# Performance work log

Hardware: AMD Instinct MI355X
Metric: run time of the kernel (lower is better)

The kernel has to match this reference:

```python
import jax, jax.numpy as jnp
import numpy as np

T, N, E, IN_DIM, HID = 3, 100000, 1600000, 128, 64


def setup_inputs() -> dict:
    key = jax.random.key(0)
    ks = jax.random.split(key, 10)
    feats = jax.random.normal(ks[0], (T, N, IN_DIM), jnp.float32)
    src_seq = jax.random.randint(ks[1], (T, E), 0, N, dtype=jnp.int32)
    dst_seq = jax.random.randint(ks[2], (T, E), 0, N, dtype=jnp.int32)
    src_next = jax.random.randint(ks[3], (E,), 0, N, dtype=jnp.int32)
    dst_next = jax.random.randint(ks[4], (E,), 0, N, dtype=jnp.int32)
    init = lambda k, shp, fan: jax.random.normal(k, shp, jnp.float32) / np.float32(np.sqrt(fan))
    W1 = init(ks[5], (IN_DIM, HID), IN_DIM)
    W2 = init(ks[6], (HID, HID), HID)
    W3 = init(ks[7], (2 * HID, HID), 2 * HID)
    W4 = init(ks[8], (HID, 1), HID)
    b1 = jnp.zeros((HID,), jnp.float32)
    b2 = jnp.zeros((HID,), jnp.float32)
    b3 = jnp.zeros((HID,), jnp.float32)
    b4 = jnp.zeros((1,), jnp.float32)
    return dict(feats=feats, W1=W1, b1=b1, W2=W2, b2=b2, W3=W3, b3=b3, W4=W4, b4=b4,
                src_seq=src_seq, dst_seq=dst_seq, src_next=src_next, dst_next=dst_next)


def _gcn_layer(x, src, dst, W, b):
    # symmetric-normalized GCN conv: h_v = (1/sqrt(d_in(v))) * sum_{u->v} x_u/sqrt(d_out(u)) @ W + b
    ones = jnp.ones(src.shape, x.dtype)
    deg_out = jax.ops.segment_sum(ones, src, num_segments=N)
    deg_in = jax.ops.segment_sum(ones, dst, num_segments=N)
    norm_src = jax.lax.rsqrt(jnp.maximum(deg_out, 1.0))
    norm_dst = jax.lax.rsqrt(jnp.maximum(deg_in, 1.0))
    msg = (x * norm_src[:, None])[src]                      # [E, d] gather
    agg = jax.ops.segment_sum(msg, dst, num_segments=N)     # [N, d] scatter-add
    agg = agg * norm_dst[:, None]
    return agg @ W + b


def _encode(x, src, dst, W1, b1, W2, b2):
    h = jax.nn.relu(_gcn_layer(x, src, dst, W1, b1))
    return _gcn_layer(h, src, dst, W2, b2)


def reference(feats, W1, b1, W2, b2, W3, b3, W4, b4, src_seq, dst_seq, src_next, dst_next):
    # per-timestep GCN encode over the T=3 snapshots (vmapped)
    h_seq = jax.vmap(lambda x, s, d: _encode(x, s, d, W1, b1, W2, b2))(feats, src_seq, dst_seq)  # [T, N, HID]
    h = h_seq[-1]  # use_temporal=False -> h_seq[:, -1, :]
    # edge gather + concat + 2-layer MLP scorer
    e = jnp.concatenate([h[src_next], h[dst_next]], axis=1)  # [E, 2*HID]
    score = jax.nn.relu(e @ W3 + b3) @ W4 + b4               # [E, 1]
    return score.squeeze(-1)
```

## Files before the change

### kernel.cpp

```cpp
#include <hip/hip_runtime.h>
#include <hip/hip_bf16.h>
#include <hip/hip_fp16.h>

#define IN_DIM 128
#define HID 64
#define BIN_BS 8192
#define BINB 512

typedef __hip_bfloat16 bf16;
typedef _Float16 fp16;
typedef _Float16 h2 __attribute__((ext_vector_type(2)));
typedef _Float16 f16x8 __attribute__((ext_vector_type(8)));
typedef float f32x4 __attribute__((ext_vector_type(4)));

__device__ __forceinline__ float loadf(const void* p, size_t i, int isf) {
    if (isf) return ((const float*)p)[i];
    unsigned int u = ((const unsigned short*)p)[i];
    union { unsigned int b; float f; } c;
    c.b = u << 16;
    return c.f;
}

__device__ __forceinline__ float bf2f(unsigned short u) {
    union { unsigned int b; float f; } c;
    c.b = ((unsigned int)u) << 16;
    return c.f;
}

__global__ void detect_kernel(const unsigned short* __restrict__ feats, int* flag) {
    int lane = threadIdx.x;
    int bad = 0;
    for (int j = lane; j < 128; j += 64) {
        unsigned short u = feats[j];
        int expo = (u >> 7) & 0xFF;
        if (expo >= 141) bad = 1;
    }
    unsigned long long m = __ballot(bad);
    if (lane == 0) *flag = (__popcll(m) > 4) ? 1 : 0;
}

__global__ void zero_kernel(int* __restrict__ p, int n) {
    int i = blockIdx.x * blockDim.x + threadIdx.x;
    int stride = gridDim.x * blockDim.x;
    for (; i < n; i += stride) p[i] = 0;
}

__global__ void gcinit_kernel(int* __restrict__ gcursor, int B, int CAP) {
    int t = blockIdx.x * blockDim.x + threadIdx.x;
    if (t < B) gcursor[t] = t * CAP;
}

__global__ __launch_bounds__(512) void bin_kernel(const int* __restrict__ src,
                                                  const int* __restrict__ dst,
                                                  int* __restrict__ deg_out,
                                                  int* __restrict__ gcursor,
                                                  int* __restrict__ binned,
                                                  int E, int sh, int nb) {
    __shared__ int scnt[BINB];
    __shared__ int sloff[BINB];
    __shared__ int sgbase[BINB];
    __shared__ int stage[BIN_BS];
    __shared__ int stotal;
    int tid = threadIdx.x;
    for (int batch = blockIdx.x; batch < nb; batch += gridDim.x) {
        int base = batch * BIN_BS;
        scnt[tid] = 0;
        __syncthreads();
        int ent[16], bk[16];
#pragma unroll
        for (int j = 0; j < 16; ++j) {
            int idx = base + tid + j * 512;
            bool ok = idx < E;
            int s = ok ? src[idx] : 0;
            int d = ok ? dst[idx] : 0;
            int b = d >> 8;
            bk[j] = ok ? b : -1;
            ent[j] = ((d & 255) << sh) | s;
            if (ok) {
                atomicAdd(&deg_out[s], 1);
                atomicAdd(&scnt[b], 1);
            }
        }
        __syncthreads();
        int c = scnt[tid];
        scnt[tid] = 0;
        sloff[tid] = c;
        __syncthreads();
        for (int off = 1; off < 512; off <<= 1) {
            int add = (tid >= off) ? sloff[tid - off] : 0;
            __syncthreads();
            sloff[tid] += add;
            __syncthreads();
        }
        int incl = sloff[tid];
        if (tid == 511) stotal = incl;
        sloff[tid] = incl - c;
        if (c > 0) sgbase[tid] = atomicAdd(&gcursor[tid], c);
        __syncthreads();
#pragma unroll
        for (int j = 0; j < 16; ++j) {
            int b = bk[j];
            if (b >= 0) {
                int r = atomicAdd(&scnt[b], 1);
                stage[sloff[b] + r] = ent[j];
            }
        }
        __syncthreads();
        int tot = stotal;
        for (int i = tid; i < tot; i += 512) {
            int lo = 0, hi = BINB - 1;
            while (lo < hi) {
                int mid = (lo + hi + 1) >> 1;
                if (sloff[mid] <= i) lo = mid;
                else hi = mid - 1;
            }
            binned[sgbase[lo] + (i - sloff[lo])] = stage[i];
        }
        __syncthreads();
    }
}

__global__ __launch_bounds__(512) void bucket_scan_kernel(const int* __restrict__ gcursor,
                                                          int* __restrict__ bbase,
                                                          int* __restrict__ row_start,
                                                          int B, int CAP, int N) {
    __shared__ int part[512];
    int tid = threadIdx.x;
    int c = (tid < B) ? (gcursor[tid] - tid * CAP) : 0;
    part[tid] = c;
    __syncthreads();
    for (int off = 1; off < 512; off <<= 1) {
        int add = (tid >= off) ? part[tid - off] : 0;
        __syncthreads();
        part[tid] += add;
        __syncthreads();
    }
    if (tid < B) bbase[tid] = part[tid] - c;
    if (tid == 511) row_start[N] = part[511];
}

__global__ __launch_bounds__(256) void csr_build_kernel(const int* __restrict__ binned,
                                                        const int* __restrict__ gcursor,
                                                        const int* __restrict__ bbase,
                                                        int* __restrict__ row_start,
                                                        int* __restrict__ csr_src,
                                                        int N, int CAP, int sh) {
    __shared__ int lcnt[256];
    __shared__ int loff[256];
    int b = blockIdx.x;
    int tid = threadIdx.x;
    int rbase = b * CAP;
    int cnt = gcursor[b] - rbase;
    int obase = bbase[b];
    int n0 = b << 8;
    int mask = (1 << sh) - 1;
    lcnt[tid] = 0;
    __syncthreads();
    for (int i = tid; i < cnt; i += 256) {
        int e = binned[rbase + i];
        atomicAdd(&lcnt[e >> sh], 1);
    }
    __syncthreads();
    int c = lcnt[tid];
    lcnt[tid] = 0;
    loff[tid] = c;
    __syncthreads();
    for (int off = 1; off < 256; off <<= 1) {
        int add = (tid >= off) ? loff[tid - off] : 0;
        __syncthreads();
        loff[tid] += add;
        __syncthreads();
    }
    int incl = loff[tid];
    loff[tid] = incl - c;
    if (n0 + tid < N) row_start[n0 + tid] = obase + incl - c;
    __syncthreads();
    for (int i = tid; i < cnt; i += 256) {
        int e = binned[rbase + i];
        int dl = e >> sh;
        int r = atomicAdd(&lcnt[dl], 1);
        csr_src[obase + loff[dl] + r] = e & mask;
    }
}


__global__ __launch_bounds__(256) void xw1_mfma_kernel(const void* __restrict__ feats, size_t xoff,
                                                       const void* __restrict__ W1,
                                                       const int* __restrict__ deg_out,
                                                       const int* __restrict__ flag,
                                                       fp16* __restrict__ y1, int N) {
    __shared__ __align__(16) fp16 Wt[HID][IN_DIM + 8];
    int isf = *flag;
    int tid = threadIdx.x;
    for (int i = tid; i < IN_DIM * HID; i += 256) {
        int k = i >> 6, c = i & 63;
        Wt[c][k] = (fp16)loadf(W1, i, isf);
    }
    __syncthreads();
    int wave = tid >> 6, lane = tid & 63;
    int lr = lane & 15;
    int lk = (lane >> 4) * 8;
    f16x8 bfr[4][4];
#pragma unroll
    for (int ct = 0; ct < 4; ++ct)
#pragma unroll
        for (int kt = 0; kt < 4; ++kt)
            bfr[ct][kt] = *(const f16x8*)&Wt[ct * 16 + lr][kt * 32 + lk];
    int tb = blockIdx.x * 64 + wave * 16;
    int rc = min(tb + lr, N - 1);
    f16x8 afr[4];
    if (isf) {
        const float* xr = (const float*)feats + xoff + (size_t)rc * IN_DIM + lk;
#pragma unroll
        for (int kt = 0; kt < 4; ++kt) {
            float4 p0 = *(const float4*)(xr + kt * 32);
            float4 p1 = *(const float4*)(xr + kt * 32 + 4);
            f16x8 a;
            a[0] = (fp16)p0.x; a[1] = (fp16)p0.y; a[2] = (fp16)p0.z; a[3] = (fp16)p0.w;
            a[4] = (fp16)p1.x; a[5] = (fp16)p1.y; a[6] = (fp16)p1.z; a[7] = (fp16)p1.w;
            afr[kt] = a;
        }
    } else {
        const unsigned short* xr = (const unsigned short*)feats + xoff + (size_t)rc * IN_DIM + lk;
#pragma unroll
        for (int kt = 0; kt < 4; ++kt) {
            uint4 q = *(const uint4*)(xr + kt * 32);
            f16x8 a;
            a[0] = (fp16)bf2f((unsigned short)(q.x & 0xffff));
            a[1] = (fp16)bf2f((unsigned short)(q.x >> 16));
            a[2] = (fp16)bf2f((unsigned short)(q.y & 0xffff));
            a[3] = (fp16)bf2f((unsigned short)(q.y >> 16));
            a[4] = (fp16)bf2f((unsigned short)(q.z & 0xffff));
            a[5] = (fp16)bf2f((unsigned short)(q.z >> 16));
            a[6] = (fp16)bf2f((unsigned short)(q.w & 0xffff));
            a[7] = (fp16)bf2f((unsigned short)(q.w >> 16));
            afr[kt] = a;
        }
    }
    f32x4 acc[4] = {};
#pragma unroll
    for (int ct = 0; ct < 4; ++ct)
#pragma unroll
        for (int kt = 0; kt < 4; ++kt)
            acc[ct] = __builtin_amdgcn_mfma_f32_16x16x32_f16(afr[kt], bfr[ct][kt], acc[ct], 0, 0, 0);
    int sr0 = tb + (lane >> 4) * 4;
    int sc = lane & 15;
#pragma unroll
    for (int i = 0; i < 4; ++i) {
        int row = sr0 + i;
        if (row < N) {
            float ns = rsqrtf(fmaxf((float)deg_out[row], 1.f));
#pragma unroll
            for (int ct = 0; ct < 4; ++ct)
                y1[(size_t)row * HID + ct * 16 + sc] = (fp16)(acc[ct][i] * ns);
        }
    }
}

__global__ __launch_bounds__(256) void mlp2_mfma_kernel(const fp16* __restrict__ h,
                                                        const void* __restrict__ W2,
                                                        const int* __restrict__ deg_out,
                                                        const int* __restrict__ flag,
                                                        fp16* __restrict__ y2, int N) {
    __shared__ __align__(16) fp16 Wt[HID][HID + 8];
    int isf = *flag;
    int tid = threadIdx.x;
    for (int i = tid; i < HID * HID; i += 256) {
        int k = i >> 6, c = i & 63;
        Wt[c][k] = (fp16)loadf(W2, i, isf);
    }
    __syncthreads();
    int wave = tid >> 6, lane = tid & 63;
    int lr = lane & 15, lk = (lane >> 4) * 8;
    f16x8 bfr[4][2];
#pragma unroll
    for (int ct = 0; ct < 4; ++ct)
#pragma unroll
        for (int kt = 0; kt < 2; ++kt)
            bfr[ct][kt] = *(const f16x8*)&Wt[ct * 16 + lr][kt * 32 + lk];
    int tb = blockIdx.x * 64 + wave * 16;
    int rc = min(tb + lr, N - 1);
    f16x8 afr[2];
#pragma unroll
    for (int kt = 0; kt < 2; ++kt)
        afr[kt] = *(const f16x8*)&h[(size_t)rc * HID + kt * 32 + lk];
    f32x4 acc[4] = {};
#pragma unroll
    for (int ct = 0; ct < 4; ++ct)
#pragma unroll
        for (int kt = 0; kt < 2; ++kt)
            acc[ct] = __builtin_amdgcn_mfma_f32_16x16x32_f16(afr[kt], bfr[ct][kt], acc[ct], 0, 0, 0);
    int sr0 = tb + (lane >> 4) * 4;
    int sc = lane & 15;
#pragma unroll
    for (int i = 0; i < 4; ++i) {
        int row = sr0 + i;
        if (row < N) {
            float ns = rsqrtf(fmaxf((float)deg_out[row], 1.f));
#pragma unroll
            for (int ct = 0; ct < 4; ++ct)
                y2[(size_t)row * HID + ct * 16 + sc] = (fp16)(acc[ct][i] * ns);
        }
    }
}

__global__ __launch_bounds__(256) void mlp3_mfma_kernel(const fp16* __restrict__ h,
                                                        const void* __restrict__ W3,
                                                        const int* __restrict__ flag,
                                                        fp16* __restrict__ u,
                                                        fp16* __restrict__ v, int N) {
    __shared__ __align__(16) fp16 Wt[HID][2 * HID + 8];
    int isf = *flag;
    int tid = threadIdx.x;
    for (int i = tid; i < 2 * HID * HID; i += 256) {
        int k = i >> 6, c = i & 63;
        Wt[c][k] = (fp16)loadf(W3, i, isf);
    }
    __syncthreads();
    int wave = tid >> 6, lane = tid & 63;
    int lr = lane & 15, lk = (lane >> 4) * 8;
    f16x8 bu[4][2], bv[4][2];
#pragma unroll
    for (int ct = 0; ct < 4; ++ct)
#pragma unroll
        for (int kt = 0; kt < 2; ++kt) {
            bu[ct][kt] = *(const f16x8*)&Wt[ct * 16 + lr][kt * 32 + lk];
            bv[ct][kt] = *(const f16x8*)&Wt[ct * 16 + lr][HID + kt * 32 + lk];
        }
    int tb = blockIdx.x * 64 + wave * 16;
    int rc = min(tb + lr, N - 1);
    f16x8 afr[2];
#pragma unroll
    for (int kt = 0; kt < 2; ++kt)
        afr[kt] = *(const f16x8*)&h[(size_t)rc * HID + kt * 32 + lk];
    f32x4 accu[4] = {}, accv[4] = {};
#pragma unroll
    for (int ct = 0; ct < 4; ++ct)
#pragma unroll
        for (int kt = 0; kt < 2; ++kt) {
            accu[ct] = __builtin_amdgcn_mfma_f32_16x16x32_f16(afr[kt], bu[ct][kt], accu[ct], 0, 0, 0);
            accv[ct] = __builtin_amdgcn_mfma_f32_16x16x32_f16(afr[kt], bv[ct][kt], accv[ct], 0, 0, 0);
        }
    int sr0 = tb + (lane >> 4) * 4;
    int sc = lane & 15;
#pragma unroll
    for (int i = 0; i < 4; ++i) {
        int row = sr0 + i;
        if (row < N) {
#pragma unroll
            for (int ct = 0; ct < 4; ++ct) {
                u[(size_t)row * HID + ct * 16 + sc] = (fp16)accu[ct][i];
                v[(size_t)row * HID + ct * 16 + sc] = (fp16)accv[ct][i];
            }
        }
    }
}

__global__ __launch_bounds__(256, 4) void gather_kernel(const fp16* __restrict__ y,
                                                        const void* __restrict__ bias,
                                                        const int* __restrict__ row_start,
                                                        const int* __restrict__ csr_src,
                                                        const int* __restrict__ flag,
                                                        fp16* __restrict__ h,
                                                        int N, int do_relu) {
    int isf = *flag;
    int tid = threadIdx.x;
    int wave = tid >> 6, lane = tid & 63;
    int half = lane >> 5, sub = lane & 31;
    float bl0 = loadf(bias, 2 * sub, isf), bl1 = loadf(bias, 2 * sub + 1, isf);
    const int NP = (N + 1) >> 1;
    for (int p = blockIdx.x * 4 + wave; p < NP; p += gridDim.x * 4) {
        int n = min(2 * p + half, N - 1);
        int rs = row_start[n];
        int re = row_start[n + 1];
        float a0 = 0.f, a1 = 0.f;
        for (int base_e = rs; base_e < re; base_e += 16) {
            int sarr[16];
#pragma unroll
            for (int j = 0; j < 16; ++j) {
                int ec = min(base_e + j, re - 1);
                sarr[j] = csr_src[ec];
            }
            unsigned uarr[16];
#pragma unroll
            for (int j = 0; j < 16; ++j)
                uarr[j] = ((const unsigned*)(y + (size_t)sarr[j] * HID))[sub];
#pragma unroll
            for (int j = 0; j < 16; ++j) {
                bool ok = base_e + j < re;
                h2 hh = __builtin_bit_cast(h2, uarr[j]);
                a0 += ok ? (float)hh[0] : 0.f;
                a1 += ok ? (float)hh[1] : 0.f;
            }
        }
        float nd = rsqrtf(fmaxf((float)(re - rs), 1.f));
        float r0 = fmaf(a0, nd, bl0);
        float r1 = fmaf(a1, nd, bl1);
        if (do_relu) { r0 = fmaxf(r0, 0.f); r1 = fmaxf(r1, 0.f); }
        if (2 * p + half < N) {
            h2 rr; rr[0] = (fp16)r0; rr[1] = (fp16)r1;
            ((unsigned*)(h + (size_t)n * HID))[sub] = __builtin_bit_cast(unsigned, rr);
        }
    }
}

#define SCORE_U 8
__global__ __launch_bounds__(256, 8) void score_kernel(const fp16* __restrict__ u,
                                                       const fp16* __restrict__ v,
                                                       const int* __restrict__ sn,
                                                       const int* __restrict__ dn,
                                                       const void* __restrict__ b3,
                                                       const void* __restrict__ W4,
                                                       const void* __restrict__ b4,
                                                       const int* __restrict__ flag,
                                                       void* __restrict__ out, int E) {
    int isf = *flag;
    int tid = threadIdx.x;
    int lane = tid & 63;
    int half = lane >> 5, sub = lane & 31;
    int gw = (blockIdx.x * 256 + tid) >> 6;
    int nw = gridDim.x * 4;
    float b30 = loadf(b3, 2 * sub, isf), b31 = loadf(b3, 2 * sub + 1, isf);
    float w40 = loadf(W4, 2 * sub, isf), w41 = loadf(W4, 2 * sub + 1, isf);
    float b4v = loadf(b4, 0, isf);
    const int P = (E + 1) >> 1;

    int p0 = gw;
    for (; p0 + (SCORE_U - 1) * nw < P - 1; p0 += SCORE_U * nw) {
        int ss[SCORE_U], dd[SCORE_U];
#pragma unroll
        for (int j = 0; j < SCORE_U; ++j) {
            int e = 2 * (p0 + j * nw) + half;
            ss[j] = sn[e];
            dd[j] = dn[e];
        }
        unsigned pu[SCORE_U], pv[SCORE_U];
#pragma unroll
        for (int j = 0; j < SCORE_U; ++j) {
            pu[j] = ((const unsigned*)(u + (size_t)ss[j] * HID))[sub];
            pv[j] = ((const unsigned*)(v + (size_t)dd[j] * HID))[sub];
        }
#pragma unroll
        for (int j = 0; j < SCORE_U; ++j) {
            int e = 2 * (p0 + j * nw) + half;
            h2 hu = __builtin_bit_cast(h2, pu[j]);
            h2 hv = __builtin_bit_cast(h2, pv[j]);
            float h0 = fmaxf((float)hu[0] + (float)hv[0] + b30, 0.f);
            float h1 = fmaxf((float)hu[1] + (float)hv[1] + b31, 0.f);
            float pp = fmaf(h0, w40, h1 * w41);
#pragma unroll
            for (int off = 16; off > 0; off >>= 1) pp += __shfl_xor(pp, off, 64);
            if (sub == 0) {
                float r = pp + b4v;
                if (isf) ((float*)out)[e] = r;
                else     ((bf16*)out)[e] = __float2bfloat16(r);
            }
        }
    }
    for (; p0 < P; p0 += nw) {
        int e = 2 * p0 + half;
        int ec = min(e, E - 1);
        int s = sn[ec], d = dn[ec];
        unsigned pu = ((const unsigned*)(u + (size_t)s * HID))[sub];
        unsigned pv = ((const unsigned*)(v + (size_t)d * HID))[sub];
        h2 hu = __builtin_bit_cast(h2, pu);
        h2 hv = __builtin_bit_cast(h2, pv);
        float h0 = fmaxf((float)hu[0] + (float)hv[0] + b30, 0.f);
        float h1 = fmaxf((float)hu[1] + (float)hv[1] + b31, 0.f);
        float pp = fmaf(h0, w40, h1 * w41);
#pragma unroll
        for (int off = 16; off > 0; off >>= 1) pp += __shfl_xor(pp, off, 64);
        if (sub == 0 && e < E) {
            float r = pp + b4v;
            if (isf) ((float*)out)[e] = r;
            else     ((bf16*)out)[e] = __float2bfloat16(r);
        }
    }
}

extern "C" void kernel_launch(void* const* d_in, const int* in_sizes, int n_in,
                              void* d_out, int out_size, void* d_ws, size_t ws_size,
                              hipStream_t stream) {
    const void* feats = d_in[0];
    const void* W1 = d_in[1];
    const void* b1 = d_in[2];
    const void* W2 = d_in[3];
    const void* b2 = d_in[4];
    const void* W3 = d_in[5];
    const void* b3 = d_in[6];
    const void* W4 = d_in[7];
    const void* b4 = d_in[8];
    const int* src_seq = (const int*)d_in[9];
    const int* dst_seq = (const int*)d_in[10];
    const int* src_next = (const int*)d_in[11];
    const int* dst_next = (const int*)d_in[12];

    const int E = in_sizes[11];
    const int N = in_sizes[0] / (3 * IN_DIM);
    const int T = in_sizes[9] / E;

    const size_t xoff = (size_t)(T - 1) * N * IN_DIM;
    const int* src = src_seq + (size_t)(T - 1) * E;
    const int* dst = dst_seq + (size_t)(T - 1) * E;

    char* w = (char*)d_ws;
    auto alloc = [&](size_t bytes) {
        void* p = (void*)w;
        w += (bytes + 255) & ~(size_t)255;
        return p;
    };
    int* flag      = (int*)alloc(4);
    int* deg_out   = (int*)alloc((size_t)N * 4);
    int* row_start = (int*)alloc((size_t)(N + 1) * 4);
    int* gcursor   = (int*)alloc(512 * 4);
    int* bbase     = (int*)alloc(512 * 4);
    int* csr_src   = (int*)alloc((size_t)E * 4);
    fp16* y1       = (fp16*)alloc((size_t)N * HID * 2);
    fp16* y2       = (fp16*)alloc((size_t)N * HID * 2);
    fp16* vv       = (fp16*)alloc((size_t)N * HID * 2);
    fp16* hbuf     = (fp16*)alloc((size_t)N * HID * 2);
    fp16* uu       = y1;
    int* binned    = (int*)y2;

    const int B = (N + 255) >> 8;
    int sh = 1;
    while ((1 << sh) < N) ++sh;
    int avg = (E + B - 1) / B;
    int CAP = (avg + avg / 2 + 256 + 15) & ~15;
    size_t maxints = (size_t)N * HID * 2 / 4;
    if ((size_t)B * CAP > maxints) CAP = (int)(maxints / B) & ~15;
    const int nb = (E + BIN_BS - 1) / BIN_BS;
    const int GB = (N + 63) / 64;

    detect_kernel<<<1, 64, 0, stream>>>((const unsigned short*)feats, flag);
    zero_kernel<<<512, 256, 0, stream>>>(deg_out, N);
    gcinit_kernel<<<2, 256, 0, stream>>>(gcursor, B, CAP);
    bin_kernel<<<nb, 512, 0, stream>>>(src, dst, deg_out, gcursor, binned, E, sh, nb);
    bucket_scan_kernel<<<1, 512, 0, stream>>>(gcursor, bbase, row_start, B, CAP, N);
    csr_build_kernel<<<B, 256, 0, stream>>>(binned, gcursor, bbase, row_start, csr_src,
                                            N, CAP, sh);
    xw1_mfma_kernel<<<GB, 256, 0, stream>>>(feats, xoff, W1, deg_out, flag, y1, N);
    gather_kernel<<<4096, 256, 0, stream>>>(y1, b1, row_start, csr_src, flag, hbuf, N, 1);
    mlp2_mfma_kernel<<<GB, 256, 0, stream>>>(hbuf, W2, deg_out, flag, y2, N);
    gather_kernel<<<4096, 256, 0, stream>>>(y2, b2, row_start, csr_src, flag, hbuf, N, 0);
    mlp3_mfma_kernel<<<GB, 256, 0, stream>>>(hbuf, W3, flag, uu, vv, N);
    score_kernel<<<4096, 256, 0, stream>>>(uu, vv, src_next, dst_next, b3, W4, b4, flag,
                                           (void*)d_out, E);
}
```

Before: 540.6 us.

## Fuse CSR neighbor gather into following MFMA matmul kernels

Each neighbor-aggregation gather is merged with the dense matmul that consumes it. The aggregated rows are staged in shared memory instead of being written to an intermediate global buffer and read back. This removes two kernel launches and the global round trip of an N×64 fp16 buffer. The separate zero and cursor-init kernels are also merged into one. In exchange, the gather now uses a fixed grid of 64-node blocks rather than a grid-stride loop, which changes load balance, and LDS use per block grows.

```diff
diff --git a/kernel.cpp b/kernel.cpp
--- a/kernel.cpp
+++ b/kernel.cpp
@@ -39,15 +39,12 @@
     if (lane == 0) *flag = (__popcll(m) > 4) ? 1 : 0;
 }
 
-__global__ void zero_kernel(int* __restrict__ p, int n) {
+__global__ void init_kernel(int* __restrict__ deg_out, int N,
+                            int* __restrict__ gcursor, int B, int CAP) {
     int i = blockIdx.x * blockDim.x + threadIdx.x;
     int stride = gridDim.x * blockDim.x;
-    for (; i < n; i += stride) p[i] = 0;
-}
-
-__global__ void gcinit_kernel(int* __restrict__ gcursor, int B, int CAP) {
-    int t = blockIdx.x * blockDim.x + threadIdx.x;
-    if (t < B) gcursor[t] = t * CAP;
+    for (int j = i; j < N; j += stride) deg_out[j] = 0;
+    if (i < B) gcursor[i] = i * CAP;
 }
 
 __global__ __launch_bounds__(512) void bin_kernel(const int* __restrict__ src,
@@ -257,20 +254,61 @@
     }
 }
 
-__global__ __launch_bounds__(256) void mlp2_mfma_kernel(const fp16* __restrict__ h,
-                                                        const void* __restrict__ W2,
-                                                        const int* __restrict__ deg_out,
-                                                        const int* __restrict__ flag,
-                                                        fp16* __restrict__ y2, int N) {
+__device__ __forceinline__ void half_gather(const fp16* __restrict__ y,
+                                            const int* __restrict__ csr_src,
+                                            int rs, int re, int sub,
+                                            float& a0, float& a1) {
+    for (int be = rs; be < re; be += 16) {
+        int sarr[16];
+#pragma unroll
+        for (int j = 0; j < 16; ++j)
+            sarr[j] = csr_src[min(be + j, re - 1)];
+        unsigned uarr[16];
+#pragma unroll
+        for (int j = 0; j < 16; ++j)
+            uarr[j] = ((const unsigned*)(y + (size_t)sarr[j] * HID))[sub];
+#pragma unroll
+        for (int j = 0; j < 16; ++j) {
+            bool ok = be + j < re;
+            h2 hh = __builtin_bit_cast(h2, uarr[j]);
+            a0 += ok ? (float)hh[0] : 0.f;
+            a1 += ok ? (float)hh[1] : 0.f;
+        }
+    }
+}
+
+__global__ __launch_bounds__(256, 4) void gmlp2_kernel(const fp16* __restrict__ y,
+                                                       const void* __restrict__ bias,
+                                                       const int* __restrict__ row_start,
+                                                       const int* __restrict__ csr_src,
+                                                       const void* __restrict__ W2,
+                                                       const int* __restrict__ deg_out,
+                                                       const int* __restrict__ flag,
+                                                       fp16* __restrict__ y2, int N) {
     __shared__ __align__(16) fp16 Wt[HID][HID + 8];
+    __shared__ __align__(16) unsigned hh[64][36];
     int isf = *flag;
     int tid = threadIdx.x;
     for (int i = tid; i < HID * HID; i += 256) {
         int k = i >> 6, c = i & 63;
         Wt[c][k] = (fp16)loadf(W2, i, isf);
     }
-    __syncthreads();
-    int wave = tid >> 6, lane = tid & 63;
+    int wave = tid >> 6, lane = tid & 63, half = lane >> 5, sub = lane & 31;
+    float bl0 = loadf(bias, 2 * sub, isf), bl1 = loadf(bias, 2 * sub + 1, isf);
+    int base_n = blockIdx.x * 64;
+    for (int it = 0; it < 8; ++it) {
+        int slot = it * 8 + wave * 2 + half;
+        int n = min(base_n + slot, N - 1);
+        int rs = row_start[n], re = row_start[n + 1];
+        float a0 = 0.f, a1 = 0.f;
+        half_gather(y, csr_src, rs, re, sub, a0, a1);
+        float nd = rsqrtf(fmaxf((float)(re - rs), 1.f));
+        h2 rr;
+        rr[0] = (fp16)fmaxf(fmaf(a0, nd, bl0), 0.f);
+        rr[1] = (fp16)fmaxf(fmaf(a1, nd, bl1), 0.f);
+        hh[slot][sub] = __builtin_bit_cast(unsigned, rr);
+    }
+    __syncthreads();
     int lr = lane & 15, lk = (lane >> 4) * 8;
     f16x8 bfr[4][2];
 #pragma unroll
@@ -278,18 +316,17 @@
 #pragma unroll
         for (int kt = 0; kt < 2; ++kt)
             bfr[ct][kt] = *(const f16x8*)&Wt[ct * 16 + lr][kt * 32 + lk];
-    int tb = blockIdx.x * 64 + wave * 16;
-    int rc = min(tb + lr, N - 1);
     f16x8 afr[2];
 #pragma unroll
     for (int kt = 0; kt < 2; ++kt)
-        afr[kt] = *(const f16x8*)&h[(size_t)rc * HID + kt * 32 + lk];
+        afr[kt] = *(const f16x8*)&hh[wave * 16 + lr][kt * 16 + (lk >> 1)];
     f32x4 acc[4] = {};
 #pragma unroll
     for (int ct = 0; ct < 4; ++ct)
 #pragma unroll
         for (int kt = 0; kt < 2; ++kt)
             acc[ct] = __builtin_amdgcn_mfma_f32_16x16x32_f16(afr[kt], bfr[ct][kt], acc[ct], 0, 0, 0);
+    int tb = base_n + wave * 16;
     int sr0 = tb + (lane >> 4) * 4;
     int sc = lane & 15;
 #pragma unroll
@@ -304,102 +341,90 @@
     }
 }
 
-__global__ __launch_bounds__(256) void mlp3_mfma_kernel(const fp16* __restrict__ h,
-                                                        const void* __restrict__ W3,
-                                                        const int* __restrict__ flag,
-                                                        fp16* __restrict__ u,
-                                                        fp16* __restrict__ v, int N) {
+__global__ __launch_bounds__(256, 4) void gmlp3_kernel(const fp16* __restrict__ y,
+                                                       const void* __restrict__ bias,
+                                                       const int* __restrict__ row_start,
+                                                       const int* __restrict__ csr_src,
+                                                       const void* __restrict__ W3,
+                                                       const int* __restrict__ flag,
+                                                       fp16* __restrict__ u,
+                                                       fp16* __restrict__ v, int N) {
     __shared__ __align__(16) fp16 Wt[HID][2 * HID + 8];
+    __shared__ __align__(16) unsigned hh[64][36];
     int isf = *flag;
     int tid = threadIdx.x;
     for (int i = tid; i < 2 * HID * HID; i += 256) {
         int k = i >> 6, c = i & 63;
         Wt[c][k] = (fp16)loadf(W3, i, isf);
     }
-    __syncthreads();
-    int wave = tid >> 6, lane = tid & 63;
+    int wave = tid >> 6, lane = tid & 63, half = lane >> 5, sub = lane & 31;
+    float bl0 = loadf(bias, 2 * sub, isf), bl1 = loadf(bias, 2 * sub + 1, isf);
+    int base_n = blockIdx.x * 64;
+    for (int it = 0; it < 8; ++it) {
+        int slot = it * 8 + wave * 2 + half;
+        int n = min(base_n + slot, N - 1);
+        int rs = row_start[n], re = row_start[n + 1];
+        float a0 = 0.f, a1 = 0.f;
+        half_gather(y, csr_src, rs, re, sub, a0, a1);
+        float nd = rsqrtf(fmaxf((float)(re - rs), 1.f));
+        h2 rr;
+        rr[0] = (fp16)fmaf(a0, nd, bl0);
+        rr[1] = (fp16)fmaf(a1, nd, bl1);
+        hh[slot][sub] = __builtin_bit_cast(unsigned, rr);
+    }
+    __syncthreads();
     int lr = lane & 15, lk = (lane >> 4) * 8;
-    f16x8 bu[4][2], bv[4][2];
-#pragma unroll
-    for (int ct = 0; ct < 4; ++ct)
-#pragma unroll
-        for (int kt = 0; kt < 2; ++kt) {
-            bu[ct][kt] = *(const f16x8*)&Wt[ct * 16 + lr][kt * 32 + lk];
-            bv[ct][kt] = *(const f16x8*)&Wt[ct * 16 + lr][HID + kt * 32 + lk];
-        }
-    int tb = blockIdx.x * 64 + wave * 16;
-    int rc = min(tb + lr, N - 1);
     f16x8 afr[2];
 #pragma unroll
     for (int kt = 0; kt < 2; ++kt)
-        afr[kt] = *(const f16x8*)&h[(size_t)rc * HID + kt * 32 + lk];
-    f32x4 accu[4] = {}, accv[4] = {};
-#pragma unroll
-    for (int ct = 0; ct < 4; ++ct)
-#pragma unroll
-        for (int kt = 0; kt < 2; ++kt) {
-            accu[ct] = __builtin_amdgcn_mfma_f32_16x16x32_f16(afr[kt], bu[ct][kt], accu[ct], 0, 0, 0);
-            accv[ct] = __builtin_amdgcn_mfma_f32_16x16x32_f16(afr[kt], bv[ct][kt], accv[ct], 0, 0, 0);
-        }
+        afr[kt] = *(const f16x8*)&hh[wave * 16 + lr][kt * 16 + (lk >> 1)];
+    int tb = base_n + wave * 16;
     int sr0 = tb + (lane >> 4) * 4;
     int sc = lane & 15;
-#pragma unroll
-    for (int i = 0; i < 4; ++i) {
-        int row = sr0 + i;
-        if (row < N) {
-#pragma unroll
-            for (int ct = 0; ct < 4; ++ct) {
-                u[(size_t)row * HID + ct * 16 + sc] = (fp16)accu[ct][i];
-                v[(size_t)row * HID + ct * 16 + sc] = (fp16)accv[ct][i];
+    {
+        f16x8 bu[4][2];
+#pragma unroll
+        for (int ct = 0; ct < 4; ++ct)
+#pragma unroll
+            for (int kt = 0; kt < 2; ++kt)
+                bu[ct][kt] = *(const f16x8*)&Wt[ct * 16 + lr][kt * 32 + lk];
+        f32x4 accu[4] = {};
+#pragma unroll
+        for (int ct = 0; ct < 4; ++ct)
+#pragma unroll
+            for (int kt = 0; kt < 2; ++kt)
+                accu[ct] = __builtin_amdgcn_mfma_f32_16x16x32_f16(afr[kt], bu[ct][kt], accu[ct], 0, 0, 0);
+#pragma unroll
+        for (int i = 0; i < 4; ++i) {
+            int row = sr0 + i;
+            if (row < N) {
+#pragma unroll
+                for (int ct = 0; ct < 4; ++ct)
+                    u[(size_t)row * HID + ct * 16 + sc] = (fp16)accu[ct][i];
             }
         }
     }
-}
-
-__global__ __launch_bounds__(256, 4) void gather_kernel(const fp16* __restrict__ y,
-                                                        const void* __restrict__ bias,
-                                                        const int* __restrict__ row_start,
-                                                        const int* __restrict__ csr_src,
-                                                        const int* __restrict__ flag,
-                                                        fp16* __restrict__ h,
-                                                        int N, int do_relu) {
-    int isf = *flag;
-    int tid = threadIdx.x;
-    int wave = tid >> 6, lane = tid & 63;
-    int half = lane >> 5, sub = lane & 31;
-    float bl0 = loadf(bias, 2 * sub, isf), bl1 = loadf(bias, 2 * sub + 1, isf);
-    const int NP = (N + 1) >> 1;
-    for (int p = blockIdx.x * 4 + wave; p < NP; p += gridDim.x * 4) {
-        int n = min(2 * p + half, N - 1);
-        int rs = row_start[n];
-        int re = row_start[n + 1];
-        float a0 = 0.f, a1 = 0.f;
-        for (int base_e = rs; base_e < re; base_e += 16) {
-            int sarr[16];
-#pragma unroll
-            for (int j = 0; j < 16; ++j) {
-                int ec = min(base_e + j, re - 1);
-                sarr[j] = csr_src[ec];
+    {
+        f16x8 bv[4][2];
+#pragma unroll
+        for (int ct = 0; ct < 4; ++ct)
+#pragma unroll
+            for (int kt = 0; kt < 2; ++kt)
+                bv[ct][kt] = *(const f16x8*)&Wt[ct * 16 + lr][HID + kt * 32 + lk];
+        f32x4 accv[4] = {};
+#pragma unroll
+        for (int ct = 0; ct < 4; ++ct)
+#pragma unroll
+            for (int kt = 0; kt < 2; ++kt)
+                accv[ct] = __builtin_amdgcn_mfma_f32_16x16x32_f16(afr[kt], bv[ct][kt], accv[ct], 0, 0, 0);
+#pragma unroll
+        for (int i = 0; i < 4; ++i) {
+            int row = sr0 + i;
+            if (row < N) {
+#pragma unroll
+                for (int ct = 0; ct < 4; ++ct)
+                    v[(size_t)row * HID + ct * 16 + sc] = (fp16)accv[ct][i];
             }
-            unsigned uarr[16];
-#pragma unroll
-            for (int j = 0; j < 16; ++j)
-                uarr[j] = ((const unsigned*)(y + (size_t)sarr[j] * HID))[sub];
-#pragma unroll
-            for (int j = 0; j < 16; ++j) {
-                bool ok = base_e + j < re;
-                h2 hh = __builtin_bit_cast(h2, uarr[j]);
-                a0 += ok ? (float)hh[0] : 0.f;
-                a1 += ok ? (float)hh[1] : 0.f;
-            }
-        }
-        float nd = rsqrtf(fmaxf((float)(re - rs), 1.f));
-        float r0 = fmaf(a0, nd, bl0);
-        float r1 = fmaf(a1, nd, bl1);
-        if (do_relu) { r0 = fmaxf(r0, 0.f); r1 = fmaxf(r1, 0.f); }
-        if (2 * p + half < N) {
-            h2 rr; rr[0] = (fp16)r0; rr[1] = (fp16)r1;
-            ((unsigned*)(h + (size_t)n * HID))[sub] = __builtin_bit_cast(unsigned, rr);
         }
     }
 }
@@ -518,7 +543,6 @@
     fp16* y1       = (fp16*)alloc((size_t)N * HID * 2);
     fp16* y2       = (fp16*)alloc((size_t)N * HID * 2);
     fp16* vv       = (fp16*)alloc((size_t)N * HID * 2);
-    fp16* hbuf     = (fp16*)alloc((size_t)N * HID * 2);
     fp16* uu       = y1;
     int* binned    = (int*)y2;
 
@@ -533,17 +557,14 @@
     const int GB = (N + 63) / 64;
 
     detect_kernel<<<1, 64, 0, stream>>>((const unsigned short*)feats, flag);
-    zero_kernel<<<512, 256, 0, stream>>>(deg_out, N);
-    gcinit_kernel<<<2, 256, 0, stream>>>(gcursor, B, CAP);
+    init_kernel<<<512, 256, 0, stream>>>(deg_out, N, gcursor, B, CAP);
     bin_kernel<<<nb, 512, 0, stream>>>(src, dst, deg_out, gcursor, binned, E, sh, nb);
     bucket_scan_kernel<<<1, 512, 0, stream>>>(gcursor, bbase, row_start, B, CAP, N);
     csr_build_kernel<<<B, 256, 0, stream>>>(binned, gcursor, bbase, row_start, csr_src,
                                             N, CAP, sh);
     xw1_mfma_kernel<<<GB, 256, 0, stream>>>(feats, xoff, W1, deg_out, flag, y1, N);
-    gather_kernel<<<4096, 256, 0, stream>>>(y1, b1, row_start, csr_src, flag, hbuf, N, 1);
-    mlp2_mfma_kernel<<<GB, 256, 0, stream>>>(hbuf, W2, deg_out, flag, y2, N);
-    gather_kernel<<<4096, 256, 0, stream>>>(y2, b2, row_start, csr_src, flag, hbuf, N, 0);
-    mlp3_mfma_kernel<<<GB, 256, 0, stream>>>(hbuf, W3, flag, uu, vv, N);
+    gmlp2_kernel<<<GB, 256, 0, stream>>>(y1, b1, row_start, csr_src, W2, deg_out, flag, y2, N);
+    gmlp3_kernel<<<GB, 256, 0, stream>>>(y2, b2, row_start, csr_src, W3, flag, uu, vv, N);
     score_kernel<<<4096, 256, 0, stream>>>(uu, vv, src_next, dst_next, b3, W4, b4, flag,
                                            (void*)d_out, E);
 }
```

Result: no change. 545.5 us (+0.9%).

## Merge init kernels and scatter binned edges directly without LDS staging

Applied to the files above, without the earlier changes.

Three tiny setup kernels (format detect, degree zeroing, cursor init) are folded into one launch to save launch overhead. The bin kernel drops its shared-memory staging buffer, prefix scan and binary-search copy-out, and writes each edge straight to its global bucket slot using the reserved base plus a shared atomic rank. This removes many barriers and LDS traffic and raises occupancy, but the global writes become scattered rather than contiguous runs, which may cost write coalescing.

```diff
diff --git a/kernel.cpp b/kernel.cpp
--- a/kernel.cpp
+++ b/kernel.cpp
@@ -27,27 +27,24 @@
     return c.f;
 }
 
-__global__ void detect_kernel(const unsigned short* __restrict__ feats, int* flag) {
-    int lane = threadIdx.x;
-    int bad = 0;
-    for (int j = lane; j < 128; j += 64) {
-        unsigned short u = feats[j];
-        int expo = (u >> 7) & 0xFF;
-        if (expo >= 141) bad = 1;
-    }
-    unsigned long long m = __ballot(bad);
-    if (lane == 0) *flag = (__popcll(m) > 4) ? 1 : 0;
-}
-
-__global__ void zero_kernel(int* __restrict__ p, int n) {
+__global__ void init_kernel(const unsigned short* __restrict__ feats, int* flag,
+                            int* __restrict__ deg_out, int N,
+                            int* __restrict__ gcursor, int B, int CAP) {
     int i = blockIdx.x * blockDim.x + threadIdx.x;
     int stride = gridDim.x * blockDim.x;
-    for (; i < n; i += stride) p[i] = 0;
-}
-
-__global__ void gcinit_kernel(int* __restrict__ gcursor, int B, int CAP) {
-    int t = blockIdx.x * blockDim.x + threadIdx.x;
-    if (t < B) gcursor[t] = t * CAP;
+    for (int j = i; j < N; j += stride) deg_out[j] = 0;
+    if (i < B) gcursor[i] = i * CAP;
+    if (blockIdx.x == 0 && threadIdx.x < 64) {
+        int lane = threadIdx.x;
+        int bad = 0;
+        for (int j = lane; j < 128; j += 64) {
+            unsigned short u = feats[j];
+            int expo = (u >> 7) & 0xFF;
+            if (expo >= 141) bad = 1;
+        }
+        unsigned long long m = __ballot(bad);
+        if (lane == 0) *flag = (__popcll(m) > 4) ? 1 : 0;
+    }
 }
 
 __global__ __launch_bounds__(512) void bin_kernel(const int* __restrict__ src,
@@ -57,10 +54,7 @@
                                                   int* __restrict__ binned,
                                                   int E, int sh, int nb) {
     __shared__ int scnt[BINB];
-    __shared__ int sloff[BINB];
     __shared__ int sgbase[BINB];
-    __shared__ int stage[BIN_BS];
-    __shared__ int stotal;
     int tid = threadIdx.x;
     for (int batch = blockIdx.x; batch < nb; batch += gridDim.x) {
         int base = batch * BIN_BS;
@@ -83,38 +77,17 @@
         }
         __syncthreads();
         int c = scnt[tid];
+        if (c > 0) sgbase[tid] = atomicAdd(&gcursor[tid], c);
+        __syncthreads();
         scnt[tid] = 0;
-        sloff[tid] = c;
-        __syncthreads();
-        for (int off = 1; off < 512; off <<= 1) {
-            int add = (tid >= off) ? sloff[tid - off] : 0;
-            __syncthreads();
-            sloff[tid] += add;
-            __syncthreads();
-        }
-        int incl = sloff[tid];
-        if (tid == 511) stotal = incl;
-        sloff[tid] = incl - c;
-        if (c > 0) sgbase[tid] = atomicAdd(&gcursor[tid], c);
         __syncthreads();
 #pragma unroll
         for (int j = 0; j < 16; ++j) {
             int b = bk[j];
             if (b >= 0) {
                 int r = atomicAdd(&scnt[b], 1);
-                stage[sloff[b] + r] = ent[j];
+                binned[sgbase[b] + r] = ent[j];
             }
-        }
-        __syncthreads();
-        int tot = stotal;
-        for (int i = tid; i < tot; i += 512) {
-            int lo = 0, hi = BINB - 1;
-            while (lo < hi) {
-                int mid = (lo + hi + 1) >> 1;
-                if (sloff[mid] <= i) lo = mid;
-                else hi = mid - 1;
-            }
-            binned[sgbase[lo] + (i - sloff[lo])] = stage[i];
         }
         __syncthreads();
     }
@@ -532,9 +505,8 @@
     const int nb = (E + BIN_BS - 1) / BIN_BS;
     const int GB = (N + 63) / 64;
 
-    detect_kernel<<<1, 64, 0, stream>>>((const unsigned short*)feats, flag);
-    zero_kernel<<<512, 256, 0, stream>>>(deg_out, N);
-    gcinit_kernel<<<2, 256, 0, stream>>>(gcursor, B, CAP);
+    init_kernel<<<512, 256, 0, stream>>>((const unsigned short*)feats, flag,
+                                         deg_out, N, gcursor, B, CAP);
     bin_kernel<<<nb, 512, 0, stream>>>(src, dst, deg_out, gcursor, binned, E, sh, nb);
     bucket_scan_kernel<<<1, 512, 0, stream>>>(gcursor, bbase, row_start, B, CAP, N);
     csr_build_kernel<<<B, 256, 0, stream>>>(binned, gcursor, bbase, row_start, csr_src,
```

New measurement: 533.9 us. Within noise of the previous version (-1.2%).
